# Performance work log

Measured on AMD Instinct MI355X. Metric: run time of the kernel, lower is better.

The kernel has to match this reference:

```python
import jax, jax.numpy as jnp
import numpy as np

N, F, C, E = 1024, 64, 4, 32768
H = 256       # MLP hidden width
C_OUT = 4     # new edge channels produced by nn_edge


def setup_inputs() -> dict:
    key = jax.random.key(0)
    ks = jax.random.split(key, 12)
    x = jax.random.normal(ks[0], (N, F), dtype=jnp.float32)
    edge_index = jax.random.randint(ks[1], (C, 2, E), 0, N)
    edge_weight = jax.random.uniform(ks[2], (C, E), dtype=jnp.float32)
    s_n1 = 1.0 / np.sqrt(C * F)
    s_n2 = 1.0 / np.sqrt(H)
    s_e1 = 1.0 / np.sqrt(C + 2 * F)
    return {
        "x": x,
        "edge_index": edge_index,
        "edge_weight": edge_weight,
        "Wn1": jax.random.normal(ks[3], (C * F, H), dtype=jnp.float32) * s_n1,
        "bn1": jnp.zeros((H,), jnp.float32),
        "Wn2": jax.random.normal(ks[4], (H, F), dtype=jnp.float32) * s_n2,
        "bn2": jnp.zeros((F,), jnp.float32),
        "We1": jax.random.normal(ks[5], (C + 2 * F, H), dtype=jnp.float32) * s_e1,
        "be1": jnp.zeros((H,), jnp.float32),
        "We2": jax.random.normal(ks[6], (H, C_OUT), dtype=jnp.float32) * s_n2,
        "be2": jnp.zeros((C_OUT,), jnp.float32),
        "eps": jnp.zeros((), jnp.float32),
    }


def reference(x, edge_index, edge_weight, Wn1, bn1, Wn2, bn2, We1, be1, We2, be2, eps):
    # ---- MCGNN: per-channel edge-weighted scatter-add aggregation ----
    def agg_one(ei, w):
        # ei: [2,E] (row0 = source j, row1 = target i); w: [E]
        msg = x[ei[0]] * w[:, None]                       # [E,F]
        return jax.ops.segment_sum(msg, ei[1], num_segments=N)  # [N,F]

    agg = jax.vmap(agg_one)(edge_index, edge_weight)      # [C,N,F]
    out_cat = agg + (1.0 + eps) * x                       # broadcast self term
    h = out_cat.transpose(1, 0, 2).reshape(N, C * F)      # [N, C*F]
    x_next = jax.nn.relu(h @ Wn1 + bn1) @ Wn2 + bn2       # [N,F]

    # ---- EDPGNN: dense adjacency per channel + broadcast x_i/x_j ----
    def dense_adj(ei, w):
        return jnp.zeros((N, N), x.dtype).at[ei[0], ei[1]].add(w)

    a = jax.vmap(dense_adj)(edge_index, edge_weight)      # [C,N,N]
    a = a.transpose(1, 2, 0)                              # [N,N,C]
    x_i = jnp.broadcast_to(x_next[:, None, :], (N, N, F))
    x_j = jnp.broadcast_to(x_next[None, :, :], (N, N, F))
    feat = jnp.concatenate([a, x_i, x_j], axis=2).reshape(N * N, C + 2 * F)
    adj_out = (jax.nn.relu(feat @ We1 + be1) @ We2 + be2).reshape(N, N, C_OUT)
    return adj_out
```

## Files before the change

kernel.cpp:

```cpp
#include <hip/hip_runtime.h>

#define NN 1024
#define FF 64
#define CC 4
#define EE 32768
#define HH 256

#define OFF_CNT1   0u
#define OFF_OFFS1  4096u
#define OFF_CUR1   8196u
#define OFF_CNT2   12292u
#define OFF_OFFS2  13316u
#define OFF_CUR2   14344u
#define OFF_SRTS   15368u
#define OFF_SRTW   146440u
#define OFF_TL     277512u
#define OFF_P      539656u
#define OFF_Q      801800u

__global__ __launch_bounds__(256)
void k_count(const int* __restrict__ ei, int* __restrict__ cnt1, int* __restrict__ cnt2)
{
    unsigned t = blockIdx.x * 256u + threadIdx.x;
    unsigned e = t & (EE - 1u);
    unsigned c = t >> 15;
    int src = ei[c * 2 * EE + e];
    int dst = ei[c * 2 * EE + EE + e];
    atomicAdd(&cnt1[c * NN + dst], 1);
    atomicAdd(&cnt2[(src >> 5) * 32 + (dst >> 5)], 1);
}

__global__ __launch_bounds__(256)
void k_scan(const int* __restrict__ cnt1, int* __restrict__ offs1, int* __restrict__ cur1,
            const int* __restrict__ cnt2, int* __restrict__ offs2, int* __restrict__ cur2)
{
    __shared__ int ws1[4], ws2[4];
    const int t = threadIdx.x;
    const int w = t >> 6;
    {
        int c[16]; int s = 0;
        const int4* cp = (const int4*)(cnt1 + t * 16);
#pragma unroll
        for (int u = 0; u < 4; ++u) {
            int4 v = cp[u];
            c[u * 4 + 0] = v.x; c[u * 4 + 1] = v.y; c[u * 4 + 2] = v.z; c[u * 4 + 3] = v.w;
            s += v.x + v.y + v.z + v.w;
        }
        int incl = s;
#pragma unroll
        for (int d = 1; d < 64; d <<= 1) {
            int v = __shfl_up(incl, d, 64);
            if ((t & 63) >= d) incl += v;
        }
        if ((t & 63) == 63) ws1[w] = incl;
        __syncthreads();
        int base = incl - s;
        for (int ww = 0; ww < w; ++ww) base += ws1[ww];
        int run = base;
#pragma unroll
        for (int u = 0; u < 16; ++u) {
            offs1[t * 16 + u] = run;
            cur1[t * 16 + u] = run;
            run += c[u];
        }
        if (t == 255) offs1[4096] = run;
    }
    __syncthreads();
    {
        int4 v = ((const int4*)cnt2)[t];
        int s = v.x + v.y + v.z + v.w;
        int incl = s;
#pragma unroll
        for (int d = 1; d < 64; d <<= 1) {
            int vv = __shfl_up(incl, d, 64);
            if ((t & 63) >= d) incl += vv;
        }
        if ((t & 63) == 63) ws2[w] = incl;
        __syncthreads();
        int base = incl - s;
        for (int ww = 0; ww < w; ++ww) base += ws2[ww];
        offs2[t * 4]     = base;             cur2[t * 4]     = base;
        offs2[t * 4 + 1] = base + v.x;       cur2[t * 4 + 1] = base + v.x;
        offs2[t * 4 + 2] = base + v.x + v.y; cur2[t * 4 + 2] = base + v.x + v.y;
        offs2[t * 4 + 3] = base + v.x + v.y + v.z;
        cur2[t * 4 + 3]  = base + v.x + v.y + v.z;
        if (t == 255) offs2[1024] = base + s;
    }
}

__global__ __launch_bounds__(256)
void k_bucket(const int* __restrict__ ei, const float* __restrict__ ew,
              int* __restrict__ cur1, int* __restrict__ srt_src, float* __restrict__ srt_w,
              int* __restrict__ cur2, int2* __restrict__ tl)
{
    unsigned t = blockIdx.x * 256u + threadIdx.x;
    unsigned e = t & (EE - 1u);
    unsigned c = t >> 15;
    int src = ei[c * 2 * EE + e];
    int dst = ei[c * 2 * EE + EE + e];
    float w = ew[c * EE + e];
    int pos1 = atomicAdd(&cur1[c * NN + dst], 1);
    srt_src[pos1] = src;
    srt_w[pos1] = w;
    int pos2 = atomicAdd(&cur2[(src >> 5) * 32 + (dst >> 5)], 1);
    tl[pos2] = make_int2((src << 12) | (dst << 2) | (int)c, __float_as_int(w));
}

__global__ __launch_bounds__(512)
void k_node(const float* __restrict__ x, const int* __restrict__ offs,
            const int* __restrict__ srt_src, const float* __restrict__ srt_w,
            const float* __restrict__ Wn1, const float* __restrict__ bn1,
            const float* __restrict__ Wn2, const float* __restrict__ bn2,
            const float* __restrict__ We1, const float* __restrict__ be1,
            const float* __restrict__ epsp,
            float* __restrict__ P, float* __restrict__ Q)
{
    __shared__ float hval[2][256];
    __shared__ float hidl[2][256];
    __shared__ float part[4][2][64];
    __shared__ float xnl[2][64];
    const int tid = threadIdx.x;
    const int n0 = blockIdx.x * 2;

    {
        const int w = tid >> 6, lane = tid & 63;
        const int c = w & 3, nn = w >> 2;
        const int g = c * NN + (n0 + nn);
        const int beg = offs[g], end = offs[g + 1];
        float acc = 0.f;
        for (int k = beg; k < end; ++k)
            acc += x[srt_src[k] * FF + lane] * srt_w[k];
        const float ope = 1.0f + epsp[0];
        hval[nn][c * 64 + lane] = acc + ope * x[(n0 + nn) * FF + lane];
    }
    __syncthreads();

    {
        const int nn = tid >> 8, h = tid & 255;
        float acc = bn1[h];
#pragma unroll 8
        for (int k = 0; k < 256; ++k)
            acc += hval[nn][k] * Wn1[k * 256 + h];
        hidl[nn][h] = fmaxf(acc, 0.f);
    }
    __syncthreads();

    {
        const int kq = tid >> 7, nn = (tid >> 6) & 1, f = tid & 63;
        float p = 0.f;
#pragma unroll 8
        for (int k = kq * 64; k < kq * 64 + 64; ++k)
            p += hidl[nn][k] * Wn2[k * 64 + f];
        part[kq][nn][f] = p;
    }
    __syncthreads();
    if (tid < 128) {
        const int nn = tid >> 6, f = tid & 63;
        xnl[nn][f] = bn2[f] + part[0][nn][f] + part[1][nn][f]
                             + part[2][nn][f] + part[3][nn][f];
    }
    __syncthreads();

    {
        const int r = tid >> 8, h = tid & 255;
        float p = be1[h], q = 0.f;
#pragma unroll 8
        for (int f = 0; f < 64; ++f) {
            float xv = xnl[r][f];
            p += xv * We1[(4 + f) * 256 + h];
            q += xv * We1[(68 + f) * 256 + h];
        }
        P[(n0 + r) * 256 + h] = p;
        Q[(n0 + r) * 256 + h] = q;
    }
}

__global__ __launch_bounds__(256, 3)
void k_edge_mlp(const float* __restrict__ P, const float* __restrict__ Q,
                const int* __restrict__ toffs, const int2* __restrict__ tl,
                const float* __restrict__ We1, const float* __restrict__ We2,
                const float* __restrict__ be2, float* __restrict__ out)
{
    __shared__ float4 aT[32 * 32];
    __shared__ float4 corr[32 * 32];
    __shared__ float4 Pl[32 * 16];
    __shared__ float4 Ql[32 * 16];
    __shared__ unsigned short list[1024];
    __shared__ int nList;

    const int tid = threadIdx.x;
    const int bi = blockIdx.y, bj = blockIdx.x;
    const int iBase = bi * 32, jBase = bj * 32;
    const int tile = bi * 32 + bj;

#pragma unroll
    for (int u = 0; u < 4; ++u) {
        aT[tid + u * 256]   = make_float4(0.f, 0.f, 0.f, 0.f);
        corr[tid + u * 256] = make_float4(0.f, 0.f, 0.f, 0.f);
    }
    if (tid == 0) nList = 0;
    __syncthreads();

    {
        const int beg = toffs[tile], n = toffs[tile + 1] - beg;
        float* aTf = (float*)aT;
        for (int k = tid; k < n; k += 256) {
            int2 ent = tl[beg + k];
            int li = (ent.x >> 12) & 31, lj = (ent.x >> 2) & 31, c = ent.x & 3;
            atomicAdd(&aTf[(li * 32 + lj) * 4 + c], __int_as_float(ent.y));
        }
    }
    __syncthreads();

#pragma unroll
    for (int u = 0; u < 4; ++u) {
        int p = tid * 4 + u;
        float4 a4 = aT[p];
        if (a4.x != 0.f || a4.y != 0.f || a4.z != 0.f || a4.w != 0.f) {
            int idx = atomicAdd(&nList, 1);
            list[idx] = (unsigned short)p;
        }
    }
    __syncthreads();
    const int nL = nList;

    const int tx = tid & 15, ty = tid >> 4;
    const int psw = ty & 7, qsw = tx & 7;

    float4 acc[2][2];
#pragma unroll
    for (int ii = 0; ii < 2; ++ii)
#pragma unroll
        for (int jj = 0; jj < 2; ++jj)
            acc[ii][jj] = make_float4(0.f, 0.f, 0.f, 0.f);

    for (int hc = 0; hc < 4; ++hc) {
#pragma unroll
        for (int u = 0; u < 2; ++u) {
            int idx = tid + u * 256;
            int row = idx >> 4, q = idx & 15;
            int ph = q ^ ((row >> 1) & 7);
            Pl[row * 16 + ph] = *(const float4*)(P + (iBase + row) * 256 + hc * 64 + q * 4);
            Ql[row * 16 + ph] = *(const float4*)(Q + (jBase + row) * 256 + hc * 64 + q * 4);
        }
        __syncthreads();

#pragma unroll 4
        for (int q = 0; q < 16; ++q) {
            float4 w2[4];
#pragma unroll
            for (int k = 0; k < 4; ++k)
                w2[k] = *(const float4*)(We2 + (hc * 64 + q * 4 + k) * 4);
            float4 p[2], qv[2];
#pragma unroll
            for (int r = 0; r < 2; ++r) p[r]  = Pl[(ty * 2 + r) * 16 + (q ^ psw)];
#pragma unroll
            for (int r = 0; r < 2; ++r) qv[r] = Ql[(tx * 2 + r) * 16 + (q ^ qsw)];
#pragma unroll
            for (int ii = 0; ii < 2; ++ii) {
#pragma unroll
                for (int jj = 0; jj < 2; ++jj) {
                    float v0 = fmaxf(p[ii].x + qv[jj].x, 0.f);
                    float v1 = fmaxf(p[ii].y + qv[jj].y, 0.f);
                    float v2 = fmaxf(p[ii].z + qv[jj].z, 0.f);
                    float v3 = fmaxf(p[ii].w + qv[jj].w, 0.f);
                    acc[ii][jj].x += v0 * w2[0].x + v1 * w2[1].x + v2 * w2[2].x + v3 * w2[3].x;
                    acc[ii][jj].y += v0 * w2[0].y + v1 * w2[1].y + v2 * w2[2].y + v3 * w2[3].y;
                    acc[ii][jj].z += v0 * w2[0].z + v1 * w2[1].z + v2 * w2[2].z + v3 * w2[3].z;
                    acc[ii][jj].w += v0 * w2[0].w + v1 * w2[1].w + v2 * w2[2].w + v3 * w2[3].w;
                }
            }
        }

        for (int en = tid; en < nL; en += 256) {
            int p = list[en];
            int li = p >> 5, lj = p & 31;
            float4 a4 = aT[p];
            float4 cc = corr[p];
            const int ps2 = (li >> 1) & 7, qs2 = (lj >> 1) & 7;
#pragma unroll 4
            for (int q = 0; q < 16; ++q) {
                float4 w1[4], w2[4];
#pragma unroll
                for (int c = 0; c < 4; ++c)
                    w1[c] = *(const float4*)(We1 + c * 256 + hc * 64 + q * 4);
#pragma unroll
                for (int k = 0; k < 4; ++k)
                    w2[k] = *(const float4*)(We2 + (hc * 64 + q * 4 + k) * 4);
                float4 pv = Pl[li * 16 + (q ^ ps2)];
                float4 qv = Ql[lj * 16 + (q ^ qs2)];
                float s0 = a4.x * w1[0].x + a4.y * w1[1].x + a4.z * w1[2].x + a4.w * w1[3].x;
                float s1 = a4.x * w1[0].y + a4.y * w1[1].y + a4.z * w1[2].y + a4.w * w1[3].y;
                float s2 = a4.x * w1[0].z + a4.y * w1[1].z + a4.z * w1[2].z + a4.w * w1[3].z;
                float s3 = a4.x * w1[0].w + a4.y * w1[1].w + a4.z * w1[2].w + a4.w * w1[3].w;
                float b0 = pv.x + qv.x, b1 = pv.y + qv.y, b2_ = pv.z + qv.z, b3 = pv.w + qv.w;
                float d0 = fmaxf(b0 + s0, 0.f) - fmaxf(b0, 0.f);
                float d1 = fmaxf(b1 + s1, 0.f) - fmaxf(b1, 0.f);
                float d2 = fmaxf(b2_ + s2, 0.f) - fmaxf(b2_, 0.f);
                float d3 = fmaxf(b3 + s3, 0.f) - fmaxf(b3, 0.f);
                cc.x += d0 * w2[0].x + d1 * w2[1].x + d2 * w2[2].x + d3 * w2[3].x;
                cc.y += d0 * w2[0].y + d1 * w2[1].y + d2 * w2[2].y + d3 * w2[3].y;
                cc.z += d0 * w2[0].z + d1 * w2[1].z + d2 * w2[2].z + d3 * w2[3].z;
                cc.w += d0 * w2[0].w + d1 * w2[1].w + d2 * w2[2].w + d3 * w2[3].w;
            }
            corr[p] = cc;
        }
        __syncthreads();
    }

    const float4 b2 = *(const float4*)be2;
#pragma unroll
    for (int ii = 0; ii < 2; ++ii)
#pragma unroll
        for (int jj = 0; jj < 2; ++jj) {
            int p = (ty * 2 + ii) * 32 + (tx * 2 + jj);
            float4 cr = corr[p];
            float4 o = acc[ii][jj];
            o.x += b2.x + cr.x; o.y += b2.y + cr.y;
            o.z += b2.z + cr.z; o.w += b2.w + cr.w;
            *(float4*)(out + ((size_t)(iBase + ty * 2 + ii) * NN + (jBase + tx * 2 + jj)) * 4) = o;
        }
}

extern "C" void kernel_launch(void* const* d_in, const int* in_sizes, int n_in,
                              void* d_out, int out_size, void* d_ws, size_t ws_size,
                              hipStream_t stream)
{
    (void)in_sizes; (void)n_in; (void)out_size; (void)ws_size;
    const float* x   = (const float*)d_in[0];
    const int*   ei  = (const int*)d_in[1];
    const float* ew  = (const float*)d_in[2];
    const float* Wn1 = (const float*)d_in[3];
    const float* bn1 = (const float*)d_in[4];
    const float* Wn2 = (const float*)d_in[5];
    const float* bn2 = (const float*)d_in[6];
    const float* We1 = (const float*)d_in[7];
    const float* be1 = (const float*)d_in[8];
    const float* We2 = (const float*)d_in[9];
    const float* be2 = (const float*)d_in[10];
    const float* eps = (const float*)d_in[11];
    float* out = (float*)d_out;

    float* ws = (float*)d_ws;
    int*   cnt1  = (int*)(ws + OFF_CNT1);
    int*   offs1 = (int*)(ws + OFF_OFFS1);
    int*   cur1  = (int*)(ws + OFF_CUR1);
    int*   cnt2  = (int*)(ws + OFF_CNT2);
    int*   offs2 = (int*)(ws + OFF_OFFS2);
    int*   cur2  = (int*)(ws + OFF_CUR2);
    int*   srts  = (int*)(ws + OFF_SRTS);
    float* srtw  = ws + OFF_SRTW;
    int2*  tl    = (int2*)(ws + OFF_TL);
    float* Pb    = ws + OFF_P;
    float* Qb    = ws + OFF_Q;

    hipMemsetAsync(d_ws, 0, (size_t)13316 * sizeof(int), stream);

    k_count <<<(CC * EE) / 256, 256, 0, stream>>>(ei, cnt1, cnt2);
    k_scan  <<<1, 256, 0, stream>>>(cnt1, offs1, cur1, cnt2, offs2, cur2);
    k_bucket<<<(CC * EE) / 256, 256, 0, stream>>>(ei, ew, cur1, srts, srtw, cur2, tl);
    k_node  <<<NN / 2, 512, 0, stream>>>(x, offs1, srts, srtw,
                                         Wn1, bn1, Wn2, bn2, We1, be1, eps, Pb, Qb);

    dim3 g(NN / 32, NN / 32);
    k_edge_mlp<<<g, 256, 0, stream>>>(Pb, Qb, offs2, tl, We1, We2, be2, out);
}
```

Before: 250.8 us.

## Fuse preprocessing into one cooperative kernel and drop the second tile bucketing

Replaces the memset, count, scan, bucket and node kernels with a single cooperative kernel that uses grid syncs and processes four nodes per block. The second per-tile edge bucketing is removed: the edge MLP kernel now rebuilds each tile's adjacency by scanning the per-destination CSR buckets and filtering on source block. Sorted source and weight are packed into int2 entries. The correction accumulators move into registers so P and Q can share one shared buffer, which lowers LDS use and allows occupancy hint 4. The trade-offs are grid-sync overhead and redundant CSR scanning, since each tile reads all edges of its 32 destination columns.

```diff
diff --git a/kernel.cpp b/kernel.cpp
--- a/kernel.cpp
+++ b/kernel.cpp
@@ -1,4 +1,7 @@
 #include <hip/hip_runtime.h>
+#include <hip/hip_cooperative_groups.h>
+
+namespace cg = cooperative_groups;
 
 #define NN 1024
 #define FF 64
@@ -6,130 +9,88 @@
 #define EE 32768
 #define HH 256
 
-#define OFF_CNT1   0u
-#define OFF_OFFS1  4096u
-#define OFF_CUR1   8196u
-#define OFF_CNT2   12292u
-#define OFF_OFFS2  13316u
-#define OFF_CUR2   14344u
-#define OFF_SRTS   15368u
-#define OFF_SRTW   146440u
-#define OFF_TL     277512u
-#define OFF_P      539656u
-#define OFF_Q      801800u
-
-__global__ __launch_bounds__(256)
-void k_count(const int* __restrict__ ei, int* __restrict__ cnt1, int* __restrict__ cnt2)
+#define OFF_CNT   0u
+#define OFF_OFFS  4096u
+#define OFF_CUR   8200u
+#define OFF_SRT   12304u
+#define OFF_P     274448u
+#define OFF_Q     536592u
+
+__global__ __launch_bounds__(1024)
+void k_pre(const float* __restrict__ x, const int* __restrict__ ei,
+           const float* __restrict__ ew,
+           const float* __restrict__ Wn1, const float* __restrict__ bn1,
+           const float* __restrict__ Wn2, const float* __restrict__ bn2,
+           const float* __restrict__ We1, const float* __restrict__ be1,
+           const float* __restrict__ epsp,
+           int* __restrict__ cnt, int* __restrict__ offs, int* __restrict__ cur,
+           int2* __restrict__ srt, float* __restrict__ P, float* __restrict__ Q)
 {
-    unsigned t = blockIdx.x * 256u + threadIdx.x;
-    unsigned e = t & (EE - 1u);
-    unsigned c = t >> 15;
-    int src = ei[c * 2 * EE + e];
-    int dst = ei[c * 2 * EE + EE + e];
-    atomicAdd(&cnt1[c * NN + dst], 1);
-    atomicAdd(&cnt2[(src >> 5) * 32 + (dst >> 5)], 1);
-}
-
-__global__ __launch_bounds__(256)
-void k_scan(const int* __restrict__ cnt1, int* __restrict__ offs1, int* __restrict__ cur1,
-            const int* __restrict__ cnt2, int* __restrict__ offs2, int* __restrict__ cur2)
-{
-    __shared__ int ws1[4], ws2[4];
-    const int t = threadIdx.x;
-    const int w = t >> 6;
-    {
-        int c[16]; int s = 0;
-        const int4* cp = (const int4*)(cnt1 + t * 16);
-#pragma unroll
-        for (int u = 0; u < 4; ++u) {
-            int4 v = cp[u];
-            c[u * 4 + 0] = v.x; c[u * 4 + 1] = v.y; c[u * 4 + 2] = v.z; c[u * 4 + 3] = v.w;
-            s += v.x + v.y + v.z + v.w;
-        }
+    cg::grid_group grid = cg::this_grid();
+    const int tid = threadIdx.x;
+    const int b = blockIdx.x;
+    const unsigned g = b * 1024u + tid;
+
+    __shared__ float hval[4][256];
+    __shared__ float hidl[4][256];
+    __shared__ float part[4][4][64];
+    __shared__ float xnl[4][64];
+    __shared__ int wsum[16];
+
+    if (g < 4096) cnt[g] = 0;
+    grid.sync();
+
+    if (g < CC * EE) {
+        unsigned e = g & (EE - 1u), c = g >> 15;
+        int dst = ei[c * 2 * EE + EE + e];
+        atomicAdd(&cnt[c * NN + dst], 1);
+    }
+    grid.sync();
+
+    if (b == 0) {
+        int4 v = ((const int4*)cnt)[tid];
+        int s = v.x + v.y + v.z + v.w;
         int incl = s;
 #pragma unroll
         for (int d = 1; d < 64; d <<= 1) {
-            int v = __shfl_up(incl, d, 64);
-            if ((t & 63) >= d) incl += v;
-        }
-        if ((t & 63) == 63) ws1[w] = incl;
+            int t2 = __shfl_up(incl, d, 64);
+            if ((tid & 63) >= d) incl += t2;
+        }
+        const int w = tid >> 6;
+        if ((tid & 63) == 63) wsum[w] = incl;
         __syncthreads();
         int base = incl - s;
-        for (int ww = 0; ww < w; ++ww) base += ws1[ww];
-        int run = base;
-#pragma unroll
-        for (int u = 0; u < 16; ++u) {
-            offs1[t * 16 + u] = run;
-            cur1[t * 16 + u] = run;
-            run += c[u];
-        }
-        if (t == 255) offs1[4096] = run;
-    }
-    __syncthreads();
-    {
-        int4 v = ((const int4*)cnt2)[t];
-        int s = v.x + v.y + v.z + v.w;
-        int incl = s;
-#pragma unroll
-        for (int d = 1; d < 64; d <<= 1) {
-            int vv = __shfl_up(incl, d, 64);
-            if ((t & 63) >= d) incl += vv;
-        }
-        if ((t & 63) == 63) ws2[w] = incl;
-        __syncthreads();
-        int base = incl - s;
-        for (int ww = 0; ww < w; ++ww) base += ws2[ww];
-        offs2[t * 4]     = base;             cur2[t * 4]     = base;
-        offs2[t * 4 + 1] = base + v.x;       cur2[t * 4 + 1] = base + v.x;
-        offs2[t * 4 + 2] = base + v.x + v.y; cur2[t * 4 + 2] = base + v.x + v.y;
-        offs2[t * 4 + 3] = base + v.x + v.y + v.z;
-        cur2[t * 4 + 3]  = base + v.x + v.y + v.z;
-        if (t == 255) offs2[1024] = base + s;
-    }
-}
-
-__global__ __launch_bounds__(256)
-void k_bucket(const int* __restrict__ ei, const float* __restrict__ ew,
-              int* __restrict__ cur1, int* __restrict__ srt_src, float* __restrict__ srt_w,
-              int* __restrict__ cur2, int2* __restrict__ tl)
-{
-    unsigned t = blockIdx.x * 256u + threadIdx.x;
-    unsigned e = t & (EE - 1u);
-    unsigned c = t >> 15;
-    int src = ei[c * 2 * EE + e];
-    int dst = ei[c * 2 * EE + EE + e];
-    float w = ew[c * EE + e];
-    int pos1 = atomicAdd(&cur1[c * NN + dst], 1);
-    srt_src[pos1] = src;
-    srt_w[pos1] = w;
-    int pos2 = atomicAdd(&cur2[(src >> 5) * 32 + (dst >> 5)], 1);
-    tl[pos2] = make_int2((src << 12) | (dst << 2) | (int)c, __float_as_int(w));
-}
-
-__global__ __launch_bounds__(512)
-void k_node(const float* __restrict__ x, const int* __restrict__ offs,
-            const int* __restrict__ srt_src, const float* __restrict__ srt_w,
-            const float* __restrict__ Wn1, const float* __restrict__ bn1,
-            const float* __restrict__ Wn2, const float* __restrict__ bn2,
-            const float* __restrict__ We1, const float* __restrict__ be1,
-            const float* __restrict__ epsp,
-            float* __restrict__ P, float* __restrict__ Q)
-{
-    __shared__ float hval[2][256];
-    __shared__ float hidl[2][256];
-    __shared__ float part[4][2][64];
-    __shared__ float xnl[2][64];
-    const int tid = threadIdx.x;
-    const int n0 = blockIdx.x * 2;
-
+        for (int ww = 0; ww < w; ++ww) base += wsum[ww];
+        offs[tid * 4]     = base;             cur[tid * 4]     = base;
+        offs[tid * 4 + 1] = base + v.x;       cur[tid * 4 + 1] = base + v.x;
+        offs[tid * 4 + 2] = base + v.x + v.y; cur[tid * 4 + 2] = base + v.x + v.y;
+        offs[tid * 4 + 3] = base + v.x + v.y + v.z;
+        cur[tid * 4 + 3]  = base + v.x + v.y + v.z;
+        if (tid == 1023) offs[4096] = base + s;
+    }
+    grid.sync();
+
+    if (g < CC * EE) {
+        unsigned e = g & (EE - 1u), c = g >> 15;
+        int src = ei[c * 2 * EE + e];
+        int dst = ei[c * 2 * EE + EE + e];
+        float w = ew[c * EE + e];
+        int pos = atomicAdd(&cur[c * NN + dst], 1);
+        srt[pos] = make_int2(src, __float_as_int(w));
+    }
+    grid.sync();
+
+    const int n0 = b * 4;
     {
         const int w = tid >> 6, lane = tid & 63;
         const int c = w & 3, nn = w >> 2;
-        const int g = c * NN + (n0 + nn);
-        const int beg = offs[g], end = offs[g + 1];
+        const int bg = c * NN + (n0 + nn);
+        const int beg = offs[bg], end = offs[bg + 1];
         float acc = 0.f;
-        for (int k = beg; k < end; ++k)
-            acc += x[srt_src[k] * FF + lane] * srt_w[k];
+        for (int k = beg; k < end; ++k) {
+            int2 e2 = srt[k];
+            acc += x[e2.x * FF + lane] * __int_as_float(e2.y);
+        }
         const float ope = 1.0f + epsp[0];
         hval[nn][c * 64 + lane] = acc + ope * x[(n0 + nn) * FF + lane];
     }
@@ -146,7 +107,7 @@
     __syncthreads();
 
     {
-        const int kq = tid >> 7, nn = (tid >> 6) & 1, f = tid & 63;
+        const int kq = tid >> 8, nn = (tid >> 6) & 3, f = tid & 63;
         float p = 0.f;
 #pragma unroll 8
         for (int k = kq * 64; k < kq * 64 + 64; ++k)
@@ -154,7 +115,7 @@
         part[kq][nn][f] = p;
     }
     __syncthreads();
-    if (tid < 128) {
+    if (tid < 256) {
         const int nn = tid >> 6, f = tid & 63;
         xnl[nn][f] = bn2[f] + part[0][nn][f] + part[1][nn][f]
                              + part[2][nn][f] + part[3][nn][f];
@@ -175,39 +136,41 @@
     }
 }
 
-__global__ __launch_bounds__(256, 3)
+__global__ __launch_bounds__(256, 4)
 void k_edge_mlp(const float* __restrict__ P, const float* __restrict__ Q,
-                const int* __restrict__ toffs, const int2* __restrict__ tl,
+                const int* __restrict__ offs, const int2* __restrict__ srt,
                 const float* __restrict__ We1, const float* __restrict__ We2,
                 const float* __restrict__ be2, float* __restrict__ out)
 {
     __shared__ float4 aT[32 * 32];
-    __shared__ float4 corr[32 * 32];
-    __shared__ float4 Pl[32 * 16];
-    __shared__ float4 Ql[32 * 16];
+    __shared__ float4 PQbuf[1024];
     __shared__ unsigned short list[1024];
     __shared__ int nList;
 
     const int tid = threadIdx.x;
     const int bi = blockIdx.y, bj = blockIdx.x;
     const int iBase = bi * 32, jBase = bj * 32;
-    const int tile = bi * 32 + bj;
-
-#pragma unroll
-    for (int u = 0; u < 4; ++u) {
-        aT[tid + u * 256]   = make_float4(0.f, 0.f, 0.f, 0.f);
-        corr[tid + u * 256] = make_float4(0.f, 0.f, 0.f, 0.f);
-    }
+
+#pragma unroll
+    for (int u = 0; u < 4; ++u)
+        aT[tid + u * 256] = make_float4(0.f, 0.f, 0.f, 0.f);
     if (tid == 0) nList = 0;
     __syncthreads();
 
     {
-        const int beg = toffs[tile], n = toffs[tile + 1] - beg;
         float* aTf = (float*)aT;
-        for (int k = tid; k < n; k += 256) {
-            int2 ent = tl[beg + k];
-            int li = (ent.x >> 12) & 31, lj = (ent.x >> 2) & 31, c = ent.x & 3;
-            atomicAdd(&aTf[(li * 32 + lj) * 4 + c], __int_as_float(ent.y));
+        const int wv = tid >> 6, lane = tid & 63;
+        for (int bkt = wv; bkt < 128; bkt += 4) {
+            const int c = bkt >> 5, dl = bkt & 31;
+            const int bg = c * NN + (jBase + dl);
+            const int beg = offs[bg], end = offs[bg + 1];
+            for (int k = beg + lane; k < end; k += 64) {
+                int2 e2 = srt[k];
+                if ((e2.x >> 5) == bi) {
+                    int li = e2.x & 31;
+                    atomicAdd(&aTf[(li * 32 + dl) * 4 + c], __int_as_float(e2.y));
+                }
+            }
         }
     }
     __syncthreads();
@@ -224,6 +187,16 @@
     __syncthreads();
     const int nL = nList;
 
+    int myp[4];
+    float4 mya[4], mycc[4];
+#pragma unroll
+    for (int k = 0; k < 4; ++k) {
+        int en = tid + k * 256;
+        if (en < nL) { myp[k] = list[en]; mya[k] = aT[myp[k]]; }
+        else         { myp[k] = -1; mya[k] = make_float4(0.f, 0.f, 0.f, 0.f); }
+        mycc[k] = make_float4(0.f, 0.f, 0.f, 0.f);
+    }
+
     const int tx = tid & 15, ty = tid >> 4;
     const int psw = ty & 7, qsw = tx & 7;
 
@@ -240,8 +213,8 @@
             int idx = tid + u * 256;
             int row = idx >> 4, q = idx & 15;
             int ph = q ^ ((row >> 1) & 7);
-            Pl[row * 16 + ph] = *(const float4*)(P + (iBase + row) * 256 + hc * 64 + q * 4);
-            Ql[row * 16 + ph] = *(const float4*)(Q + (jBase + row) * 256 + hc * 64 + q * 4);
+            PQbuf[row * 16 + ph]       = *(const float4*)(P + (iBase + row) * 256 + hc * 64 + q * 4);
+            PQbuf[512 + row * 16 + ph] = *(const float4*)(Q + (jBase + row) * 256 + hc * 64 + q * 4);
         }
         __syncthreads();
 
@@ -253,9 +226,9 @@
                 w2[k] = *(const float4*)(We2 + (hc * 64 + q * 4 + k) * 4);
             float4 p[2], qv[2];
 #pragma unroll
-            for (int r = 0; r < 2; ++r) p[r]  = Pl[(ty * 2 + r) * 16 + (q ^ psw)];
-#pragma unroll
-            for (int r = 0; r < 2; ++r) qv[r] = Ql[(tx * 2 + r) * 16 + (q ^ qsw)];
+            for (int r = 0; r < 2; ++r) p[r]  = PQbuf[(ty * 2 + r) * 16 + (q ^ psw)];
+#pragma unroll
+            for (int r = 0; r < 2; ++r) qv[r] = PQbuf[512 + (tx * 2 + r) * 16 + (q ^ qsw)];
 #pragma unroll
             for (int ii = 0; ii < 2; ++ii) {
 #pragma unroll
@@ -272,12 +245,13 @@
             }
         }
 
-        for (int en = tid; en < nL; en += 256) {
-            int p = list[en];
-            int li = p >> 5, lj = p & 31;
-            float4 a4 = aT[p];
-            float4 cc = corr[p];
+#pragma unroll
+        for (int k = 0; k < 4; ++k) {
+            if (myp[k] < 0) continue;
+            const int li = myp[k] >> 5, lj = myp[k] & 31;
             const int ps2 = (li >> 1) & 7, qs2 = (lj >> 1) & 7;
+            const float4 a4 = mya[k];
+            float4 cc = mycc[k];
 #pragma unroll 4
             for (int q = 0; q < 16; ++q) {
                 float4 w1[4], w2[4];
@@ -285,10 +259,10 @@
                 for (int c = 0; c < 4; ++c)
                     w1[c] = *(const float4*)(We1 + c * 256 + hc * 64 + q * 4);
 #pragma unroll
-                for (int k = 0; k < 4; ++k)
-                    w2[k] = *(const float4*)(We2 + (hc * 64 + q * 4 + k) * 4);
-                float4 pv = Pl[li * 16 + (q ^ ps2)];
-                float4 qv = Ql[lj * 16 + (q ^ qs2)];
+                for (int kk = 0; kk < 4; ++kk)
+                    w2[kk] = *(const float4*)(We2 + (hc * 64 + q * 4 + kk) * 4);
+                float4 pv = PQbuf[li * 16 + (q ^ ps2)];
+                float4 qv = PQbuf[512 + lj * 16 + (q ^ qs2)];
                 float s0 = a4.x * w1[0].x + a4.y * w1[1].x + a4.z * w1[2].x + a4.w * w1[3].x;
                 float s1 = a4.x * w1[0].y + a4.y * w1[1].y + a4.z * w1[2].y + a4.w * w1[3].y;
                 float s2 = a4.x * w1[0].z + a4.y * w1[1].z + a4.z * w1[2].z + a4.w * w1[3].z;
@@ -303,10 +277,20 @@
                 cc.z += d0 * w2[0].z + d1 * w2[1].z + d2 * w2[2].z + d3 * w2[3].z;
                 cc.w += d0 * w2[0].w + d1 * w2[1].w + d2 * w2[2].w + d3 * w2[3].w;
             }
-            corr[p] = cc;
+            mycc[k] = cc;
         }
         __syncthreads();
     }
+
+    float4* corr = PQbuf;
+#pragma unroll
+    for (int u = 0; u < 4; ++u)
+        corr[tid + u * 256] = make_float4(0.f, 0.f, 0.f, 0.f);
+    __syncthreads();
+#pragma unroll
+    for (int k = 0; k < 4; ++k)
+        if (myp[k] >= 0) corr[myp[k]] = mycc[k];
+    __syncthreads();
 
     const float4 b2 = *(const float4*)be2;
 #pragma unroll
@@ -342,26 +326,22 @@
     float* out = (float*)d_out;
 
     float* ws = (float*)d_ws;
-    int*   cnt1  = (int*)(ws + OFF_CNT1);
-    int*   offs1 = (int*)(ws + OFF_OFFS1);
-    int*   cur1  = (int*)(ws + OFF_CUR1);
-    int*   cnt2  = (int*)(ws + OFF_CNT2);
-    int*   offs2 = (int*)(ws + OFF_OFFS2);
-    int*   cur2  = (int*)(ws + OFF_CUR2);
-    int*   srts  = (int*)(ws + OFF_SRTS);
-    float* srtw  = ws + OFF_SRTW;
-    int2*  tl    = (int2*)(ws + OFF_TL);
-    float* Pb    = ws + OFF_P;
-    float* Qb    = ws + OFF_Q;
-
-    hipMemsetAsync(d_ws, 0, (size_t)13316 * sizeof(int), stream);
-
-    k_count <<<(CC * EE) / 256, 256, 0, stream>>>(ei, cnt1, cnt2);
-    k_scan  <<<1, 256, 0, stream>>>(cnt1, offs1, cur1, cnt2, offs2, cur2);
-    k_bucket<<<(CC * EE) / 256, 256, 0, stream>>>(ei, ew, cur1, srts, srtw, cur2, tl);
-    k_node  <<<NN / 2, 512, 0, stream>>>(x, offs1, srts, srtw,
-                                         Wn1, bn1, Wn2, bn2, We1, be1, eps, Pb, Qb);
+    int*  cnt  = (int*)(ws + OFF_CNT);
+    int*  offs = (int*)(ws + OFF_OFFS);
+    int*  cur  = (int*)(ws + OFF_CUR);
+    int2* srt  = (int2*)(ws + OFF_SRT);
+    float* Pb  = ws + OFF_P;
+    float* Qb  = ws + OFF_Q;
+
+    void* ka[] = {
+        (void*)&x, (void*)&ei, (void*)&ew,
+        (void*)&Wn1, (void*)&bn1, (void*)&Wn2, (void*)&bn2,
+        (void*)&We1, (void*)&be1, (void*)&eps,
+        (void*)&cnt, (void*)&offs, (void*)&cur, (void*)&srt,
+        (void*)&Pb, (void*)&Qb
+    };
+    hipLaunchCooperativeKernel((void*)k_pre, dim3(256), dim3(1024), ka, 0, stream);
 
     dim3 g(NN / 32, NN / 32);
-    k_edge_mlp<<<g, 256, 0, stream>>>(Pb, Qb, offs2, tl, We1, We2, be2, out);
+    k_edge_mlp<<<g, 256, 0, stream>>>(Pb, Qb, offs, srt, We1, We2, be2, out);
 }
```

Measured after the change: 321.7 us. +28.3%, slower.
